# Kernel tuning notes

Measured on AMD Instinct MI355X. Metric: run time of the kernel, lower is better.

Reference implementation:

```python
import jax, jax.numpy as jnp
import numpy as np
import math

C_S, C_Z = 384, 128
N_HEAD, C = 12, 16
N_QP, N_PV = 4, 8
B, N_RES = 1, 384


def quat_to_rot(q):
    # q: (..., 4) unnormalized quaternion -> (..., 3, 3) rotation matrix
    q = q / jnp.linalg.norm(q, axis=-1, keepdims=True)
    w, x, y, z = q[..., 0], q[..., 1], q[..., 2], q[..., 3]
    R = jnp.stack([
        1 - 2 * (y * y + z * z), 2 * (x * y - w * z), 2 * (x * z + w * y),
        2 * (x * y + w * z), 1 - 2 * (x * x + z * z), 2 * (y * z - w * x),
        2 * (x * z - w * y), 2 * (y * z + w * x), 1 - 2 * (x * x + y * y),
    ], axis=-1)
    return R.reshape(q.shape[:-1] + (3, 3))


def warp_3d_point(T, p):
    # T: (..., 1, 1, N, 4, 4) rigid transforms; p: (..., H, P, N, 3)
    R = T[..., :3, :3]
    t = T[..., :3, 3]
    return jnp.squeeze(R @ p[..., None], -1) + t


def warp_3d_point_inv(T, p):
    # Inverse rigid transform: R^T (p - t)
    R = T[..., :3, :3]
    t = T[..., :3, 3]
    return jnp.squeeze(jnp.swapaxes(R, -1, -2) @ (p - t)[..., None], -1)


def setup_inputs() -> dict:
    key = jax.random.key(0)
    ks = jax.random.split(key, 24)
    s = jax.random.normal(ks[0], (B, N_RES, C_S), dtype=jnp.float32)
    z = jax.random.normal(ks[1], (B, N_RES, N_RES, C_Z), dtype=jnp.float32)
    # Build rigid backbone transforms T (rotation from random quaternion + translation)
    quat = jax.random.normal(ks[2], (B, N_RES, 4), dtype=jnp.float32)
    trans = jax.random.normal(ks[3], (B, N_RES, 3), dtype=jnp.float32) * 10.0
    R = quat_to_rot(quat)
    T = jnp.zeros((B, N_RES, 4, 4), dtype=jnp.float32)
    T = T.at[..., :3, :3].set(R)
    T = T.at[..., :3, 3].set(trans)
    T = T.at[..., 3, 3].set(1.0)

    def lin(k, din, dout):
        kw, kb = jax.random.split(k)
        W = jax.random.normal(kw, (din, dout), dtype=jnp.float32) * 0.02
        b = jax.random.normal(kb, (dout,), dtype=jnp.float32) * 0.01
        return W, b

    Wq, bq = lin(ks[4], C_S, N_HEAD * C)
    Wk, bk = lin(ks[5], C_S, N_HEAD * C)
    Wv, bv = lin(ks[6], C_S, N_HEAD * C)
    Wqp, bqp = lin(ks[7], C_S, 3 * N_QP * N_HEAD)
    Wkp, bkp = lin(ks[8], C_S, 3 * N_QP * N_HEAD)
    Wvp, bvp = lin(ks[9], C_S, 3 * N_PV * N_HEAD)
    Wb, bb = lin(ks[10], C_Z, N_HEAD)
    d_out_in = N_HEAD * C_Z + N_HEAD * C + N_HEAD * 4 * N_PV
    Wo, bo = lin(ks[11], d_out_in, C_S)
    head_weights = jax.random.normal(ks[12], (N_HEAD,), dtype=jnp.float32) * 0.1
    return dict(s=s, z=z, T=T, Wq=Wq, bq=bq, Wk=Wk, bk=bk, Wv=Wv, bv=bv,
                Wqp=Wqp, bqp=bqp, Wkp=Wkp, bkp=bkp, Wvp=Wvp, bvp=bvp,
                Wb=Wb, bb=bb, Wo=Wo, bo=bo, head_weights=head_weights)


def ipa_forward(s, z, T, Wq, bq, Wk, bk, Wv, bv, Wqp, bqp, Wkp, bkp,
                Wvp, bvp, Wb, bb, Wo, bo, head_weights):
    batch = s.shape[:-2]
    n = s.shape[-2]
    # --- prepare qkv ---
    def heads(x):  # (..., N, H*C) -> (..., H, N, C)
        return jnp.moveaxis(x.reshape(batch + (n, N_HEAD, C)), -3, -2)
    q = heads(s @ Wq + bq)
    k = heads(s @ Wk + bk)
    v = heads(s @ Wv + bv)

    def pts(x, P):  # (..., N, 3*H*P) -> (..., H, P, N, 3)
        x = x.reshape(batch + (n, 3, N_HEAD, P))
        return jnp.moveaxis(x, (-4, -3), (-2, -1))
    qp = pts(s @ Wqp + bqp, N_QP)
    kp = pts(s @ Wkp + bkp, N_QP)
    vp = pts(s @ Wvp + bvp, N_PV)

    # --- attention scores (Alg 22 line 7) ---
    wc = math.sqrt(2.0 / (9.0 * N_QP))
    wl = math.sqrt(1.0 / 3.0)
    gamma = jax.nn.softplus(head_weights).reshape(-1, 1, 1)  # (H,1,1)
    q = q * (1.0 / math.sqrt(C))
    bias = jnp.moveaxis(z @ Wb + bb, -1, -3)  # (..., H, N, N)
    qk = jnp.einsum('...hic,...hjc->...hij', q, k)
    T_bc = T.reshape(batch + (1, 1, n, 4, 4))
    tqp = warp_3d_point(T_bc, qp)[..., :, None, :]   # (..., H, QP, N, 1, 3)
    tkp = warp_3d_point(T_bc, kp)[..., None, :, :]   # (..., H, QP, 1, N, 3)
    sq_dist = jnp.sum((tqp - tkp) ** 2, axis=-1)      # (..., H, QP, N, N)
    qpkp_term = gamma * (wc / 2.0) * jnp.sum(sq_dist, axis=-3)  # (..., H, N, N)
    att = jax.nn.softmax(wl * (qk + bias - qpkp_term), axis=-1)

    # --- outputs ---
    pairwise = jnp.einsum('...ijc,...hij->...hic', z, att)
    pairwise = jnp.moveaxis(pairwise, -3, -2).reshape(batch + (n, N_HEAD * C_Z))
    v_out = jnp.einsum('...hij,...hjc->...hic', att, v)
    v_out = jnp.moveaxis(v_out, -3, -2).reshape(batch + (n, N_HEAD * C))
    vt = warp_3d_point(T_bc, vp)                                # (..., H, PV, N, 3)
    v_att = jnp.einsum('...hij,...hkjp->...hkip', att, vt)     # (..., H, PV, N, 3)
    v_tr = warp_3d_point_inv(T_bc, v_att)                       # (..., H, PV, N, 3)
    v_tr = jnp.einsum('...hpic->...ichp', v_tr)                 # (..., N, 3, H, PV)
    norm = jnp.linalg.norm(v_tr, axis=-3, keepdims=True)        # (..., N, 1, H, PV)
    vp_norm = norm.reshape(batch + (n, N_HEAD * N_PV))
    vp_out = v_tr.reshape(batch + (n, 3 * N_HEAD * N_PV))

    out = jnp.concatenate([v_out, vp_out, vp_norm, pairwise], axis=-1)
    return out @ Wo + bo


def reference(s, z, T, Wq, bq, Wk, bk, Wv, bv, Wqp, bqp, Wkp, bkp,
              Wvp, bvp, Wb, bb, Wo, bo, head_weights):
    return ipa_forward(s, z, T, Wq, bq, Wk, bk, Wv, bv, Wqp, bqp, Wkp, bkp,
                       Wvp, bvp, Wb, bb, Wo, bo, head_weights)
```

## Files before the change

kernel.cpp:

```cpp
#include <hip/hip_runtime.h>
#include <math.h>

#define NRES 384
#define NH   12
#define WLc 0.5773502691896258f
#define WCc 0.23570226039551587f

typedef __attribute__((ext_vector_type(8))) _Float16 half8;
typedef __attribute__((ext_vector_type(4))) float f32x4;

#define OFF_P    0
#define OFF_QE   442368
#define OFF_KE   589824
#define OFF_VET  737280
#define OFF_SH   847872
#define OFF_WCT  921600
#define OFF_BCT  1142784
#define OFF_WOT  1143936
#define OFF_WBT  1549440
#define OFF_CAT  1550464

__global__ __launch_bounds__(256) void pack_kernel(
    const float* __restrict__ s,
    const float* __restrict__ Wq,  const float* __restrict__ bq,
    const float* __restrict__ Wk,  const float* __restrict__ bk,
    const float* __restrict__ Wv,  const float* __restrict__ bv,
    const float* __restrict__ Wqp, const float* __restrict__ bqp,
    const float* __restrict__ Wkp, const float* __restrict__ bkp,
    const float* __restrict__ Wvp, const float* __restrict__ bvp,
    const float* __restrict__ Wb,  const float* __restrict__ Wo,
    float* __restrict__ ws)
{
    int id = blockIdx.x * 256 + threadIdx.x;
    _Float16* sh  = (_Float16*)(ws + OFF_SH);
    _Float16* wct = (_Float16*)(ws + OFF_WCT);
    _Float16* wot = (_Float16*)(ws + OFF_WOT);
    _Float16* wbt = (_Float16*)(ws + OFF_WBT);
    float* bct = ws + OFF_BCT;

    if (id < 36864) {
        const float4 v = ((const float4*)s)[id];
        _Float16 r[4] = { (_Float16)v.x, (_Float16)v.y, (_Float16)v.z, (_Float16)v.w };
        *(uint2*)(sh + id * 4) = *(uint2*)r;
        return;
    }
    id -= 36864;
    if (id < 55296) {
        int n = id / 48, k8 = (id % 48) * 8;
        const float* W; int dout, col;
        if      (n < 192) { W = Wq;  dout = 192; col = n; }
        else if (n < 384) { W = Wk;  dout = 192; col = n - 192; }
        else if (n < 576) { W = Wv;  dout = 192; col = n - 384; }
        else if (n < 720) { W = Wqp; dout = 144; col = n - 576; }
        else if (n < 864) { W = Wkp; dout = 144; col = n - 720; }
        else              { W = Wvp; dout = 288; col = n - 864; }
        half8 r;
        #pragma unroll
        for (int j = 0; j < 8; j++) r[j] = (_Float16)W[(size_t)(k8 + j) * dout + col];
        *(half8*)(wct + (size_t)n * 384 + k8) = r;
        return;
    }
    id -= 55296;
    if (id < 101376) {
        int n = id / 264, k8 = (id % 264) * 8;
        half8 r;
        #pragma unroll
        for (int j = 0; j < 8; j++) r[j] = (_Float16)Wo[(size_t)(k8 + j) * 384 + n];
        *(half8*)(wot + (size_t)n * 2112 + k8) = r;
        return;
    }
    id -= 101376;
    if (id < 2048) {
        int h = id >> 7, c = id & 127;
        wbt[h * 128 + c] = (h < 12) ? (_Float16)(WLc * Wb[c * 12 + h]) : (_Float16)0.f;
        return;
    }
    id -= 2048;
    if (id < 1152) {
        int n = id; float b;
        if      (n < 192) b = bq[n];
        else if (n < 384) b = bk[n - 192];
        else if (n < 576) b = bv[n - 384];
        else if (n < 720) b = bqp[n - 576];
        else if (n < 864) b = bkp[n - 720];
        else              b = bvp[n - 864];
        bct[n] = b;
    }
}

__global__ __launch_bounds__(256) void proj_mfma(float* __restrict__ ws)
{
    const _Float16* sh  = (const _Float16*)(ws + OFF_SH);
    const _Float16* wct = (const _Float16*)(ws + OFF_WCT);
    const float* bct = ws + OFF_BCT;
    float* P = ws + OFF_P;

    int t = threadIdx.x, w = t >> 6, lane = t & 63;
    int m = lane & 15, q = lane >> 4;
    int n0 = blockIdx.x * 64, m0 = blockIdx.y * 64 + w * 16;

    f32x4 acc[4] = {0};
    const _Float16* arow = sh + (size_t)(m0 + m) * 384;
    #pragma unroll 4
    for (int s = 0; s < 12; s++) {
        int k = s * 32 + q * 8;
        half8 a = *(const half8*)(arow + k);
        #pragma unroll
        for (int nt = 0; nt < 4; nt++) {
            half8 b = *(const half8*)(wct + (size_t)(n0 + nt * 16 + m) * 384 + k);
            acc[nt] = __builtin_amdgcn_mfma_f32_16x16x32_f16(a, b, acc[nt], 0, 0, 0);
        }
    }
    #pragma unroll
    for (int nt = 0; nt < 4; nt++) {
        int col = n0 + nt * 16 + m;
        float bias = bct[col];
        #pragma unroll
        for (int r = 0; r < 4; r++)
            P[(size_t)(m0 + q * 4 + r) * 1152 + col] = acc[nt][r] + bias;
    }
}

__global__ __launch_bounds__(192) void prep_kernel(
    const float* __restrict__ T, const float* __restrict__ hw,
    float* __restrict__ ws)
{
    int i = blockIdx.x, t = threadIdx.x;
    const float* pr = ws + OFF_P + (size_t)i * 1152;
    float* Qe = ws + OFF_QE;
    float* Ke = ws + OFF_KE;
    _Float16* vet = (_Float16*)(ws + OFF_VET);

    __shared__ float sT[16], sG[12];
    __shared__ float sTQ[12][4][3], sTK[12][4][3];
    if (t < 16) sT[t] = T[i * 16 + t];
    if (t < 12) { float x = hw[t]; sG[t] = (x > 20.f) ? x : log1pf(__expf(x)); }
    __syncthreads();
    float R00=sT[0],R01=sT[1],R02=sT[2],t0=sT[3];
    float R10=sT[4],R11=sT[5],R12=sT[6],t1=sT[7];
    float R20=sT[8],R21=sT[9],R22=sT[10],t2=sT[11];

    if (t < 48) {
        int h = t >> 2, p = t & 3;
        float a0 = pr[576 + 0*48 + h*4 + p], a1 = pr[576 + 1*48 + h*4 + p], a2 = pr[576 + 2*48 + h*4 + p];
        sTQ[h][p][0] = R00*a0 + R01*a1 + R02*a2 + t0;
        sTQ[h][p][1] = R10*a0 + R11*a1 + R12*a2 + t1;
        sTQ[h][p][2] = R20*a0 + R21*a1 + R22*a2 + t2;
    } else if (t < 96) {
        int tt = t - 48, h = tt >> 2, p = tt & 3;
        float a0 = pr[720 + 0*48 + h*4 + p], a1 = pr[720 + 1*48 + h*4 + p], a2 = pr[720 + 2*48 + h*4 + p];
        sTK[h][p][0] = R00*a0 + R01*a1 + R02*a2 + t0;
        sTK[h][p][1] = R10*a0 + R11*a1 + R12*a2 + t1;
        sTK[h][p][2] = R20*a0 + R21*a1 + R22*a2 + t2;
    } else {
        int tt = t - 96, h = tt >> 3, p = tt & 7;
        float a0 = pr[864 + 0*96 + h*8 + p], a1 = pr[864 + 1*96 + h*8 + p], a2 = pr[864 + 2*96 + h*8 + p];
        vet[(size_t)(h*48 + 16 + p*3 + 0) * 384 + i] = (_Float16)(R00*a0 + R01*a1 + R02*a2 + t0);
        vet[(size_t)(h*48 + 16 + p*3 + 1) * 384 + i] = (_Float16)(R10*a0 + R11*a1 + R12*a2 + t1);
        vet[(size_t)(h*48 + 16 + p*3 + 2) * 384 + i] = (_Float16)(R20*a0 + R21*a1 + R22*a2 + t2);
    }
    {
        int h = t >> 4, c = t & 15;
        vet[(size_t)(h*48 + c) * 384 + i] = (_Float16)pr[384 + h*16 + c];
        if (t < 96) vet[(size_t)((t>>3)*48 + 40 + (t&7)) * 384 + i] = (_Float16)0.f;
    }
    {
        int h = t >> 4, c = t & 15;
        Qe[(size_t)i*384 + h*32 + c] = WLc * 0.25f * pr[h*16 + c];
        Ke[((size_t)h*384 + i)*32 + c] = pr[192 + h*16 + c];
    }
    __syncthreads();
    if (t < 144) {
        int h = t / 12, d = t % 12, p = d / 3, r = d % 3;
        float gw = WLc * sG[h] * WCc;
        Qe[(size_t)i*384 + h*32 + 16 + d] = gw * sTQ[h][p][r];
        Ke[((size_t)h*384 + i)*32 + 16 + d] = sTK[h][p][r];
    }
    if (t < 12) {
        int h = t;
        float sqq = 0.f, sqk = 0.f;
        #pragma unroll
        for (int p = 0; p < 4; p++)
            #pragma unroll
            for (int r = 0; r < 3; r++) { sqq += sTQ[h][p][r]*sTQ[h][p][r]; sqk += sTK[h][p][r]*sTK[h][p][r]; }
        float gw = WLc * sG[h] * WCc;
        Qe[(size_t)i*384 + h*32 + 28] = -0.5f * gw;
        Qe[(size_t)i*384 + h*32 + 29] = -0.5f * gw * sqq;
        Qe[(size_t)i*384 + h*32 + 30] = 0.f;
        Qe[(size_t)i*384 + h*32 + 31] = 0.f;
        Ke[((size_t)h*384 + i)*32 + 28] = sqk;
        Ke[((size_t)h*384 + i)*32 + 29] = 1.f;
        Ke[((size_t)h*384 + i)*32 + 30] = 0.f;
        Ke[((size_t)h*384 + i)*32 + 31] = 0.f;
    }
}

__global__ __launch_bounds__(256) void flash_kernel(
    const float* __restrict__ z, const float* __restrict__ T,
    const float* __restrict__ bb, float* __restrict__ ws)
{
    int i = blockIdx.x, t = threadIdx.x, w = t >> 6, lane = t & 63;
    int m16 = lane & 15, q = lane >> 4;

    __shared__ _Float16 zc[64 * 136];
    __shared__ _Float16 attc[16 * 72];
    __shared__ _Float16 wbl[16 * 136];
    __shared__ float bias_ch[64 * 17];
    __shared__ float sQe[384];
    __shared__ float sT[16], sBB[12], sM[12], sL[12], sAl[16], sInv[12];
    __shared__ float sO[480];

    const float* Qe = ws + OFF_QE;
    const float* Ke = ws + OFF_KE;
    const _Float16* vet = (const _Float16*)(ws + OFF_VET);
    const _Float16* wbt = (const _Float16*)(ws + OFF_WBT);
    _Float16* crow = (_Float16*)(ws + OFF_CAT) + (size_t)i * 2112;

    if (t < 16) sT[t] = T[i * 16 + t];
    if (t < 12) { sBB[t] = WLc * bb[t]; sM[t] = -1e30f; sL[t] = 0.f; }
    if (t >= 12 && t < 16) sAl[t] = 0.f;
    for (int e = t; e < 384; e += 256) sQe[e] = Qe[(size_t)i * 384 + e];
    {
        int row = t >> 4, c8 = (t & 15) * 8;
        *(half8*)(wbl + row * 136 + c8) = *(const half8*)(wbt + row * 128 + c8);
    }
    for (int e = t; e < 4 * 72; e += 256) attc[12 * 72 + e] = (_Float16)0.f;
    __syncthreads();

    f32x4 apw[2] = {0};
    float ao0 = 0.f, ao1 = 0.f;
    int h40 = t / 20, c40 = (t % 20) * 2;

    for (int ch = 0; ch < 6; ch++) {
        int j0 = ch * 64;
        __syncthreads();
        {
            int jr = t >> 2, cg = (t & 3) * 32;
            const float* zp = z + ((size_t)i * 384 + j0 + jr) * 128 + cg;
            #pragma unroll
            for (int u = 0; u < 4; u++) {
                float4 v0 = ((const float4*)zp)[u * 2];
                float4 v1 = ((const float4*)zp)[u * 2 + 1];
                half8 r;
                r[0]=(_Float16)v0.x; r[1]=(_Float16)v0.y; r[2]=(_Float16)v0.z; r[3]=(_Float16)v0.w;
                r[4]=(_Float16)v1.x; r[5]=(_Float16)v1.y; r[6]=(_Float16)v1.z; r[7]=(_Float16)v1.w;
                *(half8*)(zc + jr * 136 + cg + u * 8) = r;
            }
        }
        __syncthreads();
        {
            f32x4 bacc = {0};
            #pragma unroll
            for (int s = 0; s < 4; s++) {
                half8 a = *(const half8*)(zc + (w * 16 + m16) * 136 + s * 32 + q * 8);
                half8 b = *(const half8*)(wbl + m16 * 136 + s * 32 + q * 8);
                bacc = __builtin_amdgcn_mfma_f32_16x16x32_f16(a, b, bacc, 0, 0, 0);
            }
            #pragma unroll
            for (int r = 0; r < 4; r++)
                bias_ch[(w * 16 + q * 4 + r) * 17 + m16] = bacc[r];
        }
        __syncthreads();
        {
            #pragma unroll
            for (int u = 0; u < 3; u++) {
                int h = w * 3 + u;
                float lg = bias_ch[lane * 17 + h] + sBB[h];
                const float4* k4 = (const float4*)(Ke + ((size_t)h * 384 + j0 + lane) * 32);
                #pragma unroll
                for (int uu = 0; uu < 8; uu++) {
                    float4 kv = k4[uu];
                    lg += sQe[h*32 + uu*4 + 0] * kv.x + sQe[h*32 + uu*4 + 1] * kv.y
                        + sQe[h*32 + uu*4 + 2] * kv.z + sQe[h*32 + uu*4 + 3] * kv.w;
                }
                float mx = lg;
                #pragma unroll
                for (int off = 1; off < 64; off <<= 1) mx = fmaxf(mx, __shfl_xor(mx, off));
                float mold = sM[h];
                float mnew = fmaxf(mold, mx);
                float e = __expf(lg - mnew);
                float ssum = e;
                #pragma unroll
                for (int off = 1; off < 64; off <<= 1) ssum += __shfl_xor(ssum, off);
                float alpha = __expf(mold - mnew);
                if (lane == 0) { sM[h] = mnew; sL[h] = sL[h] * alpha + ssum; sAl[h] = alpha; }
                attc[h * 72 + lane] = (_Float16)e;
            }
        }
        __syncthreads();
        {
            float al[4];
            #pragma unroll
            for (int r = 0; r < 4; r++) al[r] = sAl[q * 4 + r];
            #pragma unroll
            for (int sub = 0; sub < 2; sub++)
                #pragma unroll
                for (int r = 0; r < 4; r++) apw[sub][r] *= al[r];
            #pragma unroll
            for (int ks = 0; ks < 2; ks++) {
                half8 a = *(const half8*)(attc + m16 * 72 + ks * 32 + q * 8);
                #pragma unroll
                for (int sub = 0; sub < 2; sub++) {
                    int c = w * 32 + sub * 16 + m16;
                    half8 b;
                    #pragma unroll
                    for (int jj = 0; jj < 8; jj++) b[jj] = zc[(ks * 32 + q * 8 + jj) * 136 + c];
                    apw[sub] = __builtin_amdgcn_mfma_f32_16x16x32_f16(a, b, apw[sub], 0, 0, 0);
                }
            }
        }
        if (t < 240) {
            float al = sAl[h40];
            float a0 = ao0 * al, a1 = ao1 * al;
            const _Float16* vp0 = vet + ((size_t)(h40 * 48 + c40)) * 384 + j0;
            const _Float16* vp1 = vp0 + 384;
            #pragma unroll
            for (int hf = 0; hf < 2; hf++) {
                half8 v0[4], v1[4];
                #pragma unroll
                for (int u = 0; u < 4; u++) {
                    v0[u] = *(const half8*)(vp0 + hf * 32 + u * 8);
                    v1[u] = *(const half8*)(vp1 + hf * 32 + u * 8);
                }
                #pragma unroll
                for (int u = 0; u < 4; u++)
                    #pragma unroll
                    for (int jj = 0; jj < 8; jj++) {
                        float av = (float)attc[h40 * 72 + hf * 32 + u * 8 + jj];
                        a0 += av * (float)v0[u][jj];
                        a1 += av * (float)v1[u][jj];
                    }
            }
            ao0 = a0; ao1 = a1;
        }
    }
    __syncthreads();
    if (t < 12) sInv[t] = 1.0f / sL[t];
    __syncthreads();
    {
        #pragma unroll
        for (int sub = 0; sub < 2; sub++)
            #pragma unroll
            for (int r = 0; r < 4; r++) {
                int h = q * 4 + r;
                if (h < 12)
                    crow[576 + h * 128 + w * 32 + sub * 16 + m16] = (_Float16)(apw[sub][r] * sInv[h]);
            }
    }
    if (t < 240) {
        sO[h40 * 40 + c40]     = ao0 * sInv[h40];
        sO[h40 * 40 + c40 + 1] = ao1 * sInv[h40];
    }
    __syncthreads();
    if (t < 192) crow[t] = (_Float16)sO[(t >> 4) * 40 + (t & 15)];
    if (t < 96) {
        int h = t >> 3, p = t & 7;
        const float* o = sO + h * 40 + 16 + p * 3;
        float x0 = o[0] - sT[3];
        float x1 = o[1] - sT[7];
        float x2 = o[2] - sT[11];
        float r0 = sT[0]*x0 + sT[4]*x1 + sT[8]*x2;
        float r1 = sT[1]*x0 + sT[5]*x1 + sT[9]*x2;
        float r2 = sT[2]*x0 + sT[6]*x1 + sT[10]*x2;
        crow[192 + 0*96 + h*8 + p] = (_Float16)r0;
        crow[192 + 1*96 + h*8 + p] = (_Float16)r1;
        crow[192 + 2*96 + h*8 + p] = (_Float16)r2;
        crow[480 + h*8 + p] = (_Float16)sqrtf(r0*r0 + r1*r1 + r2*r2);
    }
}

__global__ __launch_bounds__(256) void out_init(const float* __restrict__ bo, float* __restrict__ out)
{
    int idx = blockIdx.x * 256 + threadIdx.x;
    if (idx < 384 * 384) out[idx] = bo[idx % 384];
}

__global__ __launch_bounds__(256) void outgemm_mfma(float* __restrict__ ws, float* __restrict__ out)
{
    const _Float16* catb = (const _Float16*)(ws + OFF_CAT);
    const _Float16* wot  = (const _Float16*)(ws + OFF_WOT);

    int t = threadIdx.x, w = t >> 6, lane = t & 63;
    int m = lane & 15, q = lane >> 4;
    int n0 = blockIdx.x * 64, m0 = blockIdx.y * 64 + w * 16;
    int kbase = blockIdx.z * 704;

    f32x4 acc[4] = {0};
    const _Float16* arow = catb + (size_t)(m0 + m) * 2112;
    #pragma unroll 2
    for (int s = 0; s < 22; s++) {
        int k = kbase + s * 32 + q * 8;
        half8 a = *(const half8*)(arow + k);
        #pragma unroll
        for (int nt = 0; nt < 4; nt++) {
            half8 b = *(const half8*)(wot + (size_t)(n0 + nt * 16 + m) * 2112 + k);
            acc[nt] = __builtin_amdgcn_mfma_f32_16x16x32_f16(a, b, acc[nt], 0, 0, 0);
        }
    }
    #pragma unroll
    for (int nt = 0; nt < 4; nt++) {
        int col = n0 + nt * 16 + m;
        #pragma unroll
        for (int r = 0; r < 4; r++)
            atomicAdd(&out[(size_t)(m0 + q * 4 + r) * 384 + col], acc[nt][r]);
    }
}

extern "C" void kernel_launch(void* const* d_in, const int* in_sizes, int n_in,
                              void* d_out, int out_size, void* d_ws, size_t ws_size,
                              hipStream_t stream)
{
    const float* s   = (const float*)d_in[0];
    const float* z   = (const float*)d_in[1];
    const float* T   = (const float*)d_in[2];
    const float* Wq  = (const float*)d_in[3];
    const float* bq  = (const float*)d_in[4];
    const float* Wk  = (const float*)d_in[5];
    const float* bk  = (const float*)d_in[6];
    const float* Wv  = (const float*)d_in[7];
    const float* bv  = (const float*)d_in[8];
    const float* Wqp = (const float*)d_in[9];
    const float* bqp = (const float*)d_in[10];
    const float* Wkp = (const float*)d_in[11];
    const float* bkp = (const float*)d_in[12];
    const float* Wvp = (const float*)d_in[13];
    const float* bvp = (const float*)d_in[14];
    const float* Wb  = (const float*)d_in[15];
    const float* bb  = (const float*)d_in[16];
    const float* Wo  = (const float*)d_in[17];
    const float* bo  = (const float*)d_in[18];
    const float* hw  = (const float*)d_in[19];
    float* ws  = (float*)d_ws;
    float* out = (float*)d_out;

    pack_kernel<<<769, 256, 0, stream>>>(s, Wq, bq, Wk, bk, Wv, bv,
                                         Wqp, bqp, Wkp, bkp, Wvp, bvp, Wb, Wo, ws);
    proj_mfma<<<dim3(18, 6), 256, 0, stream>>>(ws);
    prep_kernel<<<384, 192, 0, stream>>>(T, hw, ws);
    flash_kernel<<<384, 256, 0, stream>>>(z, T, bb, ws);
    out_init<<<576, 256, 0, stream>>>(bo, out);
    outgemm_mfma<<<dim3(6, 6, 3), 256, 0, stream>>>(ws, out);
}
```

Before: 252.4 us.

## Replace online-softmax flash kernel with full-row softmax and split value/point epilogue

The chunked online-softmax attention kernel becomes a one-pass kernel per query row. It computes all 384 pair biases via MFMA directly from global z, then runs a full softmax, writes fp16 attention to the workspace, and does the pair-feature MFMA reading z straight from global memory. A new kernel computes the scalar and point value outputs with MFMA from the stored attention, followed by the inverse-frame epilogue. The weight-packing transposes now go through shared-memory tiles for coalesced access. The output GEMM drops the split-K atomics and separate bias-init kernel, writing bias plus result directly. z is now read twice from global memory, with strided, uncoalesced fp32 loads in the pair-feature pass, and an extra attention buffer round-trips through memory.

Result: slower. 287.0 us (+13.7%).

```diff
diff --git a/kernel.cpp b/kernel.cpp
--- a/kernel.cpp
+++ b/kernel.cpp
@@ -19,6 +19,7 @@
 #define OFF_WOT  1143936
 #define OFF_WBT  1549440
 #define OFF_CAT  1550464
+#define OFF_ATT  1955968
 
 __global__ __launch_bounds__(256) void pack_kernel(
     const float* __restrict__ s,
@@ -31,60 +32,84 @@
     const float* __restrict__ Wb,  const float* __restrict__ Wo,
     float* __restrict__ ws)
 {
-    int id = blockIdx.x * 256 + threadIdx.x;
+    int b = blockIdx.x, t = threadIdx.x;
     _Float16* sh  = (_Float16*)(ws + OFF_SH);
     _Float16* wct = (_Float16*)(ws + OFF_WCT);
     _Float16* wot = (_Float16*)(ws + OFF_WOT);
     _Float16* wbt = (_Float16*)(ws + OFF_WBT);
     float* bct = ws + OFF_BCT;
 
-    if (id < 36864) {
-        const float4 v = ((const float4*)s)[id];
+    if (b < 144) {
+        int id = b * 256 + t;
+        float4 v = ((const float4*)s)[id];
         _Float16 r[4] = { (_Float16)v.x, (_Float16)v.y, (_Float16)v.z, (_Float16)v.w };
         *(uint2*)(sh + id * 4) = *(uint2*)r;
         return;
     }
-    id -= 36864;
-    if (id < 55296) {
-        int n = id / 48, k8 = (id % 48) * 8;
+    __shared__ float tile[64 * 65];
+    if (b < 252) {
+        int ti = b - 144;
+        int k0 = (ti % 6) * 64, n0 = (ti / 6) * 64;
+        int cl = t & 63, rg = t >> 6;
+        int ncat = n0 + cl;
         const float* W; int dout, col;
-        if      (n < 192) { W = Wq;  dout = 192; col = n; }
-        else if (n < 384) { W = Wk;  dout = 192; col = n - 192; }
-        else if (n < 576) { W = Wv;  dout = 192; col = n - 384; }
-        else if (n < 720) { W = Wqp; dout = 144; col = n - 576; }
-        else if (n < 864) { W = Wkp; dout = 144; col = n - 720; }
-        else              { W = Wvp; dout = 288; col = n - 864; }
-        half8 r;
-        #pragma unroll
-        for (int j = 0; j < 8; j++) r[j] = (_Float16)W[(size_t)(k8 + j) * dout + col];
-        *(half8*)(wct + (size_t)n * 384 + k8) = r;
+        if      (ncat < 192) { W = Wq;  dout = 192; col = ncat; }
+        else if (ncat < 384) { W = Wk;  dout = 192; col = ncat - 192; }
+        else if (ncat < 576) { W = Wv;  dout = 192; col = ncat - 384; }
+        else if (ncat < 720) { W = Wqp; dout = 144; col = ncat - 576; }
+        else if (ncat < 864) { W = Wkp; dout = 144; col = ncat - 720; }
+        else                 { W = Wvp; dout = 288; col = ncat - 864; }
+        #pragma unroll
+        for (int u = 0; u < 16; u++) {
+            int r = rg * 16 + u;
+            tile[r * 65 + cl] = W[(size_t)(k0 + r) * dout + col];
+        }
+        __syncthreads();
+        #pragma unroll
+        for (int u2 = 0; u2 < 2; u2++) {
+            int item = t + 256 * u2;
+            int nl = item >> 3, kg = item & 7;
+            half8 rr;
+            #pragma unroll
+            for (int jj = 0; jj < 8; jj++) rr[jj] = (_Float16)tile[(kg * 8 + jj) * 65 + nl];
+            *(half8*)(wct + (size_t)(n0 + nl) * 384 + k0 + kg * 8) = rr;
+        }
         return;
     }
-    id -= 55296;
-    if (id < 101376) {
-        int n = id / 264, k8 = (id % 264) * 8;
-        half8 r;
-        #pragma unroll
-        for (int j = 0; j < 8; j++) r[j] = (_Float16)Wo[(size_t)(k8 + j) * 384 + n];
-        *(half8*)(wot + (size_t)n * 2112 + k8) = r;
+    if (b < 450) {
+        int ti = b - 252;
+        int k0 = (ti % 33) * 64, n0 = (ti / 33) * 64;
+        int cl = t & 63, rg = t >> 6;
+        #pragma unroll
+        for (int u = 0; u < 16; u++) {
+            int r = rg * 16 + u;
+            tile[r * 65 + cl] = Wo[(size_t)(k0 + r) * 384 + n0 + cl];
+        }
+        __syncthreads();
+        #pragma unroll
+        for (int u2 = 0; u2 < 2; u2++) {
+            int item = t + 256 * u2;
+            int nl = item >> 3, kg = item & 7;
+            half8 rr;
+            #pragma unroll
+            for (int jj = 0; jj < 8; jj++) rr[jj] = (_Float16)tile[(kg * 8 + jj) * 65 + nl];
+            *(half8*)(wot + (size_t)(n0 + nl) * 2112 + k0 + kg * 8) = rr;
+        }
         return;
     }
-    id -= 101376;
-    if (id < 2048) {
-        int h = id >> 7, c = id & 127;
+    for (int e = t; e < 2048; e += 256) {
+        int h = e >> 7, c = e & 127;
         wbt[h * 128 + c] = (h < 12) ? (_Float16)(WLc * Wb[c * 12 + h]) : (_Float16)0.f;
-        return;
-    }
-    id -= 2048;
-    if (id < 1152) {
-        int n = id; float b;
-        if      (n < 192) b = bq[n];
-        else if (n < 384) b = bk[n - 192];
-        else if (n < 576) b = bv[n - 384];
-        else if (n < 720) b = bqp[n - 576];
-        else if (n < 864) b = bkp[n - 720];
-        else              b = bvp[n - 864];
-        bct[n] = b;
+    }
+    for (int e = t; e < 1152; e += 256) {
+        float bv_;
+        if      (e < 192) bv_ = bq[e];
+        else if (e < 384) bv_ = bk[e - 192];
+        else if (e < 576) bv_ = bv[e - 384];
+        else if (e < 720) bv_ = bqp[e - 576];
+        else if (e < 864) bv_ = bkp[e - 720];
+        else              bv_ = bvp[e - 864];
+        bct[e] = bv_;
     }
 }
 
@@ -163,9 +188,6 @@
         int h = t >> 4, c = t & 15;
         vet[(size_t)(h*48 + c) * 384 + i] = (_Float16)pr[384 + h*16 + c];
         if (t < 96) vet[(size_t)((t>>3)*48 + 40 + (t&7)) * 384 + i] = (_Float16)0.f;
-    }
-    {
-        int h = t >> 4, c = t & 15;
         Qe[(size_t)i*384 + h*32 + c] = WLc * 0.25f * pr[h*16 + c];
         Ke[((size_t)h*384 + i)*32 + c] = pr[192 + h*16 + c];
     }
@@ -195,187 +217,179 @@
     }
 }
 
-__global__ __launch_bounds__(256) void flash_kernel(
-    const float* __restrict__ z, const float* __restrict__ T,
-    const float* __restrict__ bb, float* __restrict__ ws)
+__global__ __launch_bounds__(256) void attn_fused(
+    const float* __restrict__ z, const float* __restrict__ bb,
+    float* __restrict__ ws)
 {
     int i = blockIdx.x, t = threadIdx.x, w = t >> 6, lane = t & 63;
     int m16 = lane & 15, q = lane >> 4;
 
-    __shared__ _Float16 zc[64 * 136];
-    __shared__ _Float16 attc[16 * 72];
+    __shared__ float sBias[384 * 13];
+    __shared__ _Float16 sAtt[16 * 392];
     __shared__ _Float16 wbl[16 * 136];
-    __shared__ float bias_ch[64 * 17];
     __shared__ float sQe[384];
-    __shared__ float sT[16], sBB[12], sM[12], sL[12], sAl[16], sInv[12];
-    __shared__ float sO[480];
+    __shared__ float sBB[12];
 
     const float* Qe = ws + OFF_QE;
     const float* Ke = ws + OFF_KE;
-    const _Float16* vet = (const _Float16*)(ws + OFF_VET);
     const _Float16* wbt = (const _Float16*)(ws + OFF_WBT);
+    _Float16* attg = (_Float16*)(ws + OFF_ATT);
     _Float16* crow = (_Float16*)(ws + OFF_CAT) + (size_t)i * 2112;
-
-    if (t < 16) sT[t] = T[i * 16 + t];
-    if (t < 12) { sBB[t] = WLc * bb[t]; sM[t] = -1e30f; sL[t] = 0.f; }
-    if (t >= 12 && t < 16) sAl[t] = 0.f;
-    for (int e = t; e < 384; e += 256) sQe[e] = Qe[(size_t)i * 384 + e];
+    const float* zrow = z + (size_t)i * 384 * 128;
+
+    if (t < 12) sBB[t] = WLc * bb[t];
     {
         int row = t >> 4, c8 = (t & 15) * 8;
         *(half8*)(wbl + row * 136 + c8) = *(const half8*)(wbt + row * 128 + c8);
     }
-    for (int e = t; e < 4 * 72; e += 256) attc[12 * 72 + e] = (_Float16)0.f;
-    __syncthreads();
-
-    f32x4 apw[2] = {0};
-    float ao0 = 0.f, ao1 = 0.f;
-    int h40 = t / 20, c40 = (t % 20) * 2;
-
-    for (int ch = 0; ch < 6; ch++) {
-        int j0 = ch * 64;
-        __syncthreads();
-        {
-            int jr = t >> 2, cg = (t & 3) * 32;
-            const float* zp = z + ((size_t)i * 384 + j0 + jr) * 128 + cg;
-            #pragma unroll
-            for (int u = 0; u < 4; u++) {
-                float4 v0 = ((const float4*)zp)[u * 2];
-                float4 v1 = ((const float4*)zp)[u * 2 + 1];
-                half8 r;
-                r[0]=(_Float16)v0.x; r[1]=(_Float16)v0.y; r[2]=(_Float16)v0.z; r[3]=(_Float16)v0.w;
-                r[4]=(_Float16)v1.x; r[5]=(_Float16)v1.y; r[6]=(_Float16)v1.z; r[7]=(_Float16)v1.w;
-                *(half8*)(zc + jr * 136 + cg + u * 8) = r;
-            }
-        }
-        __syncthreads();
-        {
-            f32x4 bacc = {0};
-            #pragma unroll
-            for (int s = 0; s < 4; s++) {
-                half8 a = *(const half8*)(zc + (w * 16 + m16) * 136 + s * 32 + q * 8);
-                half8 b = *(const half8*)(wbl + m16 * 136 + s * 32 + q * 8);
-                bacc = __builtin_amdgcn_mfma_f32_16x16x32_f16(a, b, bacc, 0, 0, 0);
-            }
+    for (int e = t; e < 4 * 392; e += 256) sAtt[12 * 392 + e] = (_Float16)0.f;
+    for (int e = t; e < 384; e += 256) sQe[e] = Qe[(size_t)i * 384 + e];
+    __syncthreads();
+
+    #pragma unroll
+    for (int u = 0; u < 6; u++) {
+        int j = (w + 4 * u) * 16 + m16;
+        const float* zp = zrow + (size_t)j * 128 + q * 8;
+        f32x4 acc = {0.f, 0.f, 0.f, 0.f};
+        #pragma unroll
+        for (int s = 0; s < 4; s++) {
+            float4 v0 = *(const float4*)(zp + s * 32);
+            float4 v1 = *(const float4*)(zp + s * 32 + 4);
+            half8 a;
+            a[0]=(_Float16)v0.x; a[1]=(_Float16)v0.y; a[2]=(_Float16)v0.z; a[3]=(_Float16)v0.w;
+            a[4]=(_Float16)v1.x; a[5]=(_Float16)v1.y; a[6]=(_Float16)v1.z; a[7]=(_Float16)v1.w;
+            half8 b = *(const half8*)(wbl + m16 * 136 + s * 32 + q * 8);
+            acc = __builtin_amdgcn_mfma_f32_16x16x32_f16(a, b, acc, 0, 0, 0);
+        }
+        if (m16 < 12) {
             #pragma unroll
             for (int r = 0; r < 4; r++)
-                bias_ch[(w * 16 + q * 4 + r) * 17 + m16] = bacc[r];
-        }
-        __syncthreads();
-        {
+                sBias[((w + 4 * u) * 16 + q * 4 + r) * 13 + m16] = acc[r];
+        }
+    }
+    __syncthreads();
+
+    for (int j = t; j < 384; j += 256) {
+        #pragma unroll
+        for (int h = 0; h < 12; h++) {
+            const float4* k4 = (const float4*)(Ke + ((size_t)h * 384 + j) * 32);
+            float dot = 0.f;
             #pragma unroll
-            for (int u = 0; u < 3; u++) {
-                int h = w * 3 + u;
-                float lg = bias_ch[lane * 17 + h] + sBB[h];
-                const float4* k4 = (const float4*)(Ke + ((size_t)h * 384 + j0 + lane) * 32);
-                #pragma unroll
-                for (int uu = 0; uu < 8; uu++) {
-                    float4 kv = k4[uu];
-                    lg += sQe[h*32 + uu*4 + 0] * kv.x + sQe[h*32 + uu*4 + 1] * kv.y
-                        + sQe[h*32 + uu*4 + 2] * kv.z + sQe[h*32 + uu*4 + 3] * kv.w;
-                }
-                float mx = lg;
-                #pragma unroll
-                for (int off = 1; off < 64; off <<= 1) mx = fmaxf(mx, __shfl_xor(mx, off));
-                float mold = sM[h];
-                float mnew = fmaxf(mold, mx);
-                float e = __expf(lg - mnew);
-                float ssum = e;
-                #pragma unroll
-                for (int off = 1; off < 64; off <<= 1) ssum += __shfl_xor(ssum, off);
-                float alpha = __expf(mold - mnew);
-                if (lane == 0) { sM[h] = mnew; sL[h] = sL[h] * alpha + ssum; sAl[h] = alpha; }
-                attc[h * 72 + lane] = (_Float16)e;
+            for (int uu = 0; uu < 8; uu++) {
+                float4 kv = k4[uu];
+                dot += sQe[h*32+uu*4+0]*kv.x + sQe[h*32+uu*4+1]*kv.y
+                     + sQe[h*32+uu*4+2]*kv.z + sQe[h*32+uu*4+3]*kv.w;
             }
-        }
-        __syncthreads();
-        {
-            float al[4];
-            #pragma unroll
-            for (int r = 0; r < 4; r++) al[r] = sAl[q * 4 + r];
-            #pragma unroll
-            for (int sub = 0; sub < 2; sub++)
-                #pragma unroll
-                for (int r = 0; r < 4; r++) apw[sub][r] *= al[r];
-            #pragma unroll
-            for (int ks = 0; ks < 2; ks++) {
-                half8 a = *(const half8*)(attc + m16 * 72 + ks * 32 + q * 8);
-                #pragma unroll
-                for (int sub = 0; sub < 2; sub++) {
-                    int c = w * 32 + sub * 16 + m16;
-                    half8 b;
-                    #pragma unroll
-                    for (int jj = 0; jj < 8; jj++) b[jj] = zc[(ks * 32 + q * 8 + jj) * 136 + c];
-                    apw[sub] = __builtin_amdgcn_mfma_f32_16x16x32_f16(a, b, apw[sub], 0, 0, 0);
-                }
-            }
-        }
-        if (t < 240) {
-            float al = sAl[h40];
-            float a0 = ao0 * al, a1 = ao1 * al;
-            const _Float16* vp0 = vet + ((size_t)(h40 * 48 + c40)) * 384 + j0;
-            const _Float16* vp1 = vp0 + 384;
-            #pragma unroll
-            for (int hf = 0; hf < 2; hf++) {
-                half8 v0[4], v1[4];
-                #pragma unroll
-                for (int u = 0; u < 4; u++) {
-                    v0[u] = *(const half8*)(vp0 + hf * 32 + u * 8);
-                    v1[u] = *(const half8*)(vp1 + hf * 32 + u * 8);
-                }
-                #pragma unroll
-                for (int u = 0; u < 4; u++)
-                    #pragma unroll
-                    for (int jj = 0; jj < 8; jj++) {
-                        float av = (float)attc[h40 * 72 + hf * 32 + u * 8 + jj];
-                        a0 += av * (float)v0[u][jj];
-                        a1 += av * (float)v1[u][jj];
-                    }
-            }
-            ao0 = a0; ao1 = a1;
-        }
-    }
-    __syncthreads();
-    if (t < 12) sInv[t] = 1.0f / sL[t];
-    __syncthreads();
-    {
-        #pragma unroll
-        for (int sub = 0; sub < 2; sub++)
-            #pragma unroll
-            for (int r = 0; r < 4; r++) {
-                int h = q * 4 + r;
-                if (h < 12)
-                    crow[576 + h * 128 + w * 32 + sub * 16 + m16] = (_Float16)(apw[sub][r] * sInv[h]);
-            }
-    }
-    if (t < 240) {
-        sO[h40 * 40 + c40]     = ao0 * sInv[h40];
-        sO[h40 * 40 + c40 + 1] = ao1 * sInv[h40];
-    }
-    __syncthreads();
-    if (t < 192) crow[t] = (_Float16)sO[(t >> 4) * 40 + (t & 15)];
-    if (t < 96) {
-        int h = t >> 3, p = t & 7;
-        const float* o = sO + h * 40 + 16 + p * 3;
-        float x0 = o[0] - sT[3];
-        float x1 = o[1] - sT[7];
-        float x2 = o[2] - sT[11];
-        float r0 = sT[0]*x0 + sT[4]*x1 + sT[8]*x2;
-        float r1 = sT[1]*x0 + sT[5]*x1 + sT[9]*x2;
-        float r2 = sT[2]*x0 + sT[6]*x1 + sT[10]*x2;
-        crow[192 + 0*96 + h*8 + p] = (_Float16)r0;
-        crow[192 + 1*96 + h*8 + p] = (_Float16)r1;
-        crow[192 + 2*96 + h*8 + p] = (_Float16)r2;
-        crow[480 + h*8 + p] = (_Float16)sqrtf(r0*r0 + r1*r1 + r2*r2);
-    }
-}
-
-__global__ __launch_bounds__(256) void out_init(const float* __restrict__ bo, float* __restrict__ out)
-{
-    int idx = blockIdx.x * 256 + threadIdx.x;
-    if (idx < 384 * 384) out[idx] = bo[idx % 384];
-}
-
-__global__ __launch_bounds__(256) void outgemm_mfma(float* __restrict__ ws, float* __restrict__ out)
+            sBias[j * 13 + h] = sBias[j * 13 + h] + sBB[h] + dot;
+        }
+    }
+    __syncthreads();
+
+    #pragma unroll
+    for (int u = 0; u < 3; u++) {
+        int h = w * 3 + u;
+        float v[6], mx = -1e30f;
+        #pragma unroll
+        for (int g = 0; g < 6; g++) { v[g] = sBias[(lane + 64*g) * 13 + h]; mx = fmaxf(mx, v[g]); }
+        #pragma unroll
+        for (int off = 1; off < 64; off <<= 1) mx = fmaxf(mx, __shfl_xor(mx, off));
+        float sm = 0.f;
+        #pragma unroll
+        for (int g = 0; g < 6; g++) { v[g] = __expf(v[g] - mx); sm += v[g]; }
+        #pragma unroll
+        for (int off = 1; off < 64; off <<= 1) sm += __shfl_xor(sm, off);
+        float inv = 1.0f / sm;
+        #pragma unroll
+        for (int g = 0; g < 6; g++) {
+            _Float16 a = (_Float16)(v[g] * inv);
+            sAtt[h * 392 + lane + 64 * g] = a;
+            attg[((size_t)h * 384 + i) * 384 + lane + 64 * g] = a;
+        }
+    }
+    __syncthreads();
+
+    f32x4 apw0 = {0}, apw1 = {0};
+    #pragma unroll 3
+    for (int s = 0; s < 12; s++) {
+        int k = s * 32 + q * 8;
+        half8 a = *(const half8*)(sAtt + m16 * 392 + k);
+        const float* zp = zrow + (size_t)k * 128 + w * 32 + m16;
+        half8 b0, b1;
+        #pragma unroll
+        for (int jj = 0; jj < 8; jj++) {
+            b0[jj] = (_Float16)zp[(size_t)jj * 128];
+            b1[jj] = (_Float16)zp[(size_t)jj * 128 + 16];
+        }
+        apw0 = __builtin_amdgcn_mfma_f32_16x16x32_f16(a, b0, apw0, 0, 0, 0);
+        apw1 = __builtin_amdgcn_mfma_f32_16x16x32_f16(a, b1, apw1, 0, 0, 0);
+    }
+    if (q < 3) {
+        #pragma unroll
+        for (int r = 0; r < 4; r++) {
+            int h = q * 4 + r;
+            crow[576 + h * 128 + w * 32 + m16]      = (_Float16)apw0[r];
+            crow[576 + h * 128 + w * 32 + 16 + m16] = (_Float16)apw1[r];
+        }
+    }
+}
+
+__global__ __launch_bounds__(128) void out40_ep(
+    const float* __restrict__ T, float* __restrict__ ws)
+{
+    const _Float16* attg = (const _Float16*)(ws + OFF_ATT);
+    const _Float16* vet  = (const _Float16*)(ws + OFF_VET);
+    _Float16* catb = (_Float16*)(ws + OFF_CAT);
+
+    int h = blockIdx.y, t = threadIdx.x, w = t >> 6, lane = t & 63;
+    int m16 = lane & 15, q = lane >> 4;
+    int i0 = blockIdx.x * 32;
+
+    __shared__ float sO[32 * 49];
+    __shared__ float sTT[32 * 17];
+    for (int e = t; e < 512; e += 128)
+        sTT[(e >> 4) * 17 + (e & 15)] = T[(size_t)(i0 + (e >> 4)) * 16 + (e & 15)];
+
+    f32x4 acc[3] = {0};
+    const _Float16* arow = attg + ((size_t)h * 384 + i0 + w * 16 + m16) * 384;
+    #pragma unroll 3
+    for (int s = 0; s < 12; s++) {
+        int k = s * 32 + q * 8;
+        half8 a = *(const half8*)(arow + k);
+        #pragma unroll
+        for (int nt = 0; nt < 3; nt++) {
+            half8 b = *(const half8*)(vet + (size_t)(h * 48 + nt * 16 + m16) * 384 + k);
+            acc[nt] = __builtin_amdgcn_mfma_f32_16x16x32_f16(a, b, acc[nt], 0, 0, 0);
+        }
+    }
+    #pragma unroll
+    for (int nt = 0; nt < 3; nt++)
+        #pragma unroll
+        for (int r = 0; r < 4; r++)
+            sO[(w * 16 + q * 4 + r) * 49 + nt * 16 + m16] = acc[nt][r];
+    __syncthreads();
+
+    for (int e = t; e < 512; e += 128) {
+        int il = e >> 4, c = e & 15;
+        catb[(size_t)(i0 + il) * 2112 + h * 16 + c] = (_Float16)sO[il * 49 + c];
+    }
+    for (int e = t; e < 256; e += 128) {
+        int il = e >> 3, p = e & 7;
+        const float* o = sO + il * 49 + 16 + p * 3;
+        const float* Ti = sTT + il * 17;
+        float x0 = o[0] - Ti[3], x1 = o[1] - Ti[7], x2 = o[2] - Ti[11];
+        float r0 = Ti[0]*x0 + Ti[4]*x1 + Ti[8]*x2;
+        float r1 = Ti[1]*x0 + Ti[5]*x1 + Ti[9]*x2;
+        float r2 = Ti[2]*x0 + Ti[6]*x1 + Ti[10]*x2;
+        _Float16* cr = catb + (size_t)(i0 + il) * 2112;
+        cr[192 + 0*96 + h*8 + p] = (_Float16)r0;
+        cr[192 + 1*96 + h*8 + p] = (_Float16)r1;
+        cr[192 + 2*96 + h*8 + p] = (_Float16)r2;
+        cr[480 + h*8 + p] = (_Float16)sqrtf(r0*r0 + r1*r1 + r2*r2);
+    }
+}
+
+__global__ __launch_bounds__(256) void outgemm_mfma(
+    const float* __restrict__ bo, float* __restrict__ ws, float* __restrict__ out)
 {
     const _Float16* catb = (const _Float16*)(ws + OFF_CAT);
     const _Float16* wot  = (const _Float16*)(ws + OFF_WOT);
@@ -383,13 +397,12 @@
     int t = threadIdx.x, w = t >> 6, lane = t & 63;
     int m = lane & 15, q = lane >> 4;
     int n0 = blockIdx.x * 64, m0 = blockIdx.y * 64 + w * 16;
-    int kbase = blockIdx.z * 704;
 
     f32x4 acc[4] = {0};
     const _Float16* arow = catb + (size_t)(m0 + m) * 2112;
     #pragma unroll 2
-    for (int s = 0; s < 22; s++) {
-        int k = kbase + s * 32 + q * 8;
+    for (int s = 0; s < 66; s++) {
+        int k = s * 32 + q * 8;
         half8 a = *(const half8*)(arow + k);
         #pragma unroll
         for (int nt = 0; nt < 4; nt++) {
@@ -400,9 +413,10 @@
     #pragma unroll
     for (int nt = 0; nt < 4; nt++) {
         int col = n0 + nt * 16 + m;
+        float bias = bo[col];
         #pragma unroll
         for (int r = 0; r < 4; r++)
-            atomicAdd(&out[(size_t)(m0 + q * 4 + r) * 384 + col], acc[nt][r]);
+            out[(size_t)(m0 + q * 4 + r) * 384 + col] = acc[nt][r] + bias;
     }
 }
 
@@ -433,11 +447,11 @@
     float* ws  = (float*)d_ws;
     float* out = (float*)d_out;
 
-    pack_kernel<<<769, 256, 0, stream>>>(s, Wq, bq, Wk, bk, Wv, bv,
+    pack_kernel<<<451, 256, 0, stream>>>(s, Wq, bq, Wk, bk, Wv, bv,
                                          Wqp, bqp, Wkp, bkp, Wvp, bvp, Wb, Wo, ws);
     proj_mfma<<<dim3(18, 6), 256, 0, stream>>>(ws);
     prep_kernel<<<384, 192, 0, stream>>>(T, hw, ws);
-    flash_kernel<<<384, 256, 0, stream>>>(z, T, bb, ws);
-    out_init<<<576, 256, 0, stream>>>(bo, out);
-    outgemm_mfma<<<dim3(6, 6, 3), 256, 0, stream>>>(ws, out);
-}
+    attn_fused<<<384, 256, 0, stream>>>(z, bb, ws);
+    out40_ep<<<dim3(12, 12), 128, 0, stream>>>(T, ws);
+    outgemm_mfma<<<dim3(6, 6), 256, 0, stream>>>(bo, ws, out);
+}
```
